# Kernel optimization log

Measured on AMD Instinct MI355X. Metric: run time of the kernel, lower is better.

Reference implementation:

```python
import jax, jax.numpy as jnp
import numpy as np

BN_EPS = 1e-5


def _weight_mlp(off, Wh, bh, Wo, bo):
    # off: [Nout, k, 2] relative neighbor offsets -> [Nout, k, 9] interp coeffs
    h = jax.nn.relu(off @ Wh + bh)
    return h @ Wo + bo


def _interp_conv(x, idx, off, Wk, bk, Wh, bh, Wo, bo):
    # x: [B, Cin, Nin]; idx: [Nout, k] neighbor indices into Nin; Wk: [Cout, Cin, 9]
    a = _weight_mlp(off, Wh, bh, Wo, bo)        # [Nout, k, 9]
    feats = x[:, :, idx]                         # gather -> [B, Cin, Nout, k]
    # dynamic filter: per-neighbor kernel = a @ Wk taps, contracted with features
    y = jnp.einsum('nkt,bcnk,oct->bon', a, feats, Wk)  # [B, Cout, Nout]
    return y + bk[None, :, None]


def _bn_relu(x, g, b):
    # BatchNorm1d over [B, C, N] using batch statistics (training-mode forward)
    mean = x.mean(axis=(0, 2), keepdims=True)
    var = x.var(axis=(0, 2), keepdims=True)
    xn = (x - mean) * jax.lax.rsqrt(var + BN_EPS)
    return jax.nn.relu(xn * g[None, :, None] + b[None, :, None])


def setup_inputs() -> dict:
    key = jax.random.key(0)
    ks = jax.random.split(key, 12)
    B, N1, N2, N3, K = 8, 50176, 12544, 3136, 9
    inp = {
        'x': jax.random.normal(ks[0], (B, 3, N1), jnp.float32),
        'nbr1': jax.random.randint(ks[1], (N2, K), 0, N1, jnp.int32),
        'off1': jax.random.normal(ks[2], (N2, K, 2), jnp.float32),
        'nbr2': jax.random.randint(ks[3], (N2, K), 0, N2, jnp.int32),
        'off2': jax.random.normal(ks[4], (N2, K, 2), jnp.float32),
        'pool_idx': jax.random.randint(ks[5], (N3, K), 0, N2, jnp.int32),
        'Wh': jax.random.normal(ks[6], (2, 32), jnp.float32) * 0.5,
        'bh': jnp.zeros((32,), jnp.float32),
        'Wo': jax.random.normal(ks[7], (32, 9), jnp.float32) * 0.2,
        'bo': jnp.zeros((9,), jnp.float32),
        'W1': jax.random.normal(ks[8], (32, 3, 9), jnp.float32) * 0.2,
        'b1': jnp.zeros((32,), jnp.float32),
        'W2': jax.random.normal(ks[9], (32, 32, 9), jnp.float32) * 0.06,
        'b2': jnp.zeros((32,), jnp.float32),
        'W3': jax.random.normal(ks[10], (64, 32, 9), jnp.float32) * 0.06,
        'b3': jnp.zeros((64,), jnp.float32),
        'g1': jnp.ones((32,), jnp.float32), 'be1': jnp.zeros((32,), jnp.float32),
        'g2': jnp.ones((32,), jnp.float32), 'be2': jnp.zeros((32,), jnp.float32),
        'g3': jnp.ones((64,), jnp.float32), 'be3': jnp.zeros((64,), jnp.float32),
    }
    return inp


def reference(x, nbr1, off1, nbr2, off2, pool_idx, Wh, bh, Wo, bo,
              W1, b1, W2, b2, W3, b3, g1, be1, g2, be2, g3, be3):
    x = _bn_relu(_interp_conv(x, nbr1, off1, W1, b1, Wh, bh, Wo, bo), g1, be1)
    x = _bn_relu(_interp_conv(x, nbr2, off2, W2, b2, Wh, bh, Wo, bo), g2, be2)
    x = _bn_relu(_interp_conv(x, nbr2, off2, W3, b3, Wh, bh, Wo, bo), g3, be3)
    # MaxPoolNG: max over irregular neighbor sets from level l2 -> l3
    x = x[:, :, pool_idx].max(axis=-1)           # [B, 64, N3]
    return x
```

## Files before the change

kernel.cpp:

```cpp
#include <hip/hip_runtime.h>
#include <math.h>

#define N1C 50176
#define N2C 12544
#define N3C 3136
#define NT_TILES (N2C * 8 / 64)

typedef __attribute__((ext_vector_type(8))) short bf16x8;
typedef __attribute__((ext_vector_type(4))) float f32x4;

__device__ __forceinline__ unsigned short f2bf(float f) {
    unsigned u = __builtin_bit_cast(unsigned, f);
    u += 0x7fffu + ((u >> 16) & 1u);
    return (unsigned short)(u >> 16);
}
__device__ __forceinline__ unsigned packbf(float a, float b) {
    return (unsigned)f2bf(a) | ((unsigned)f2bf(b) << 16);
}
__device__ __forceinline__ float bf2f(unsigned short u) {
    return __builtin_bit_cast(float, (unsigned)u << 16);
}
__device__ __forceinline__ float bflo(unsigned u) {
    return __builtin_bit_cast(float, u << 16);
}
__device__ __forceinline__ float bfhi(unsigned u) {
    return __builtin_bit_cast(float, u & 0xffff0000u);
}

#define TRB (N1C / 64)
#define MLB (2 * N2C * 9 / 256)
#define PWB 112

__device__ __forceinline__ void pad_one(int i, const float* __restrict__ W,
                                        unsigned short* __restrict__ Wp,
                                        int OC, int CIN, int KT) {
    int j = i & 7;
    int op = (i >> 3) & 31;
    int q = (i >> 8) & 3;
    int kt = (i >> 10) % KT;
    int g = i / (KT * 1024);
    int kp = kt * 32 + q * 8 + j;
    int t = kp / CIN, c = kp - t * CIN;
    int o = g * 32 + op;
    float v = (t < 9 && o < OC) ? W[(o * CIN + c) * 9 + t] : 0.f;
    Wp[i] = f2bf(v);
}

__global__ void prologue_kernel(const float* __restrict__ x, unsigned short* __restrict__ X0,
                                const float* __restrict__ off1, const float* __restrict__ off2,
                                const float* __restrict__ Wh, const float* __restrict__ bh,
                                const float* __restrict__ Wo, const float* __restrict__ bo,
                                float* __restrict__ A1, float* __restrict__ A2,
                                const float* __restrict__ W1, const float* __restrict__ W2,
                                const float* __restrict__ W3,
                                unsigned short* __restrict__ W1p, unsigned short* __restrict__ W2p,
                                unsigned short* __restrict__ W3p) {
    __shared__ float T[64][25];
    int blk = blockIdx.x;
    int tid = threadIdx.x;
    if (blk < TRB) {
        int n0 = blk * 64;
        for (int r = tid; r < 24 * 64; r += 256) {
            int cb = r >> 6;
            int nn = r & 63;
            T[nn][cb] = x[cb * N1C + n0 + nn];
        }
        __syncthreads();
        for (int w = tid; w < 64 * 24; w += 256) {
            int nn = w / 24;
            int u = w - nn * 24;
            X0[(n0 + nn) * 24 + u] = f2bf(T[nn][u]);
        }
    } else if (blk < TRB + MLB) {
        int idx = (blk - TRB) * 256 + tid;
        const float* offp;
        float* Ap;
        if (idx < N2C * 9) { offp = off1 + idx * 2; Ap = A1 + idx * 9; }
        else { int i2 = idx - N2C * 9; offp = off2 + i2 * 2; Ap = A2 + i2 * 9; }
        float o0 = offp[0], o1 = offp[1];
        float out[9];
#pragma unroll
        for (int t = 0; t < 9; t++) out[t] = bo[t];
#pragma unroll
        for (int h = 0; h < 32; h++) {
            float hv = fmaxf(o0 * Wh[h] + o1 * Wh[32 + h] + bh[h], 0.f);
#pragma unroll
            for (int t = 0; t < 9; t++) out[t] += hv * Wo[h * 9 + t];
        }
#pragma unroll
        for (int t = 0; t < 9; t++) Ap[t] = out[t];
    } else {
        int i = (blk - TRB - MLB) * 256 + tid;
        if (i < 1024) pad_one(i, W1, W1p, 32, 3, 1);
        else if (i < 10240) pad_one(i - 1024, W2, W2p, 32, 32, 9);
        else pad_one(i - 10240, W3, W3p, 64, 288 / 9, 9);
    }
}

template <int CIN, int MW, bool HAS_BN>
__global__ __launch_bounds__(256, 4)
void conv_kernel(const unsigned short* __restrict__ Xin,
                 const int* __restrict__ nbr,
                 const float* __restrict__ A,
                 const unsigned short* __restrict__ Wp,
                 const float* __restrict__ bias,
                 const float* __restrict__ bnsc,
                 const float* __restrict__ bnsh,
                 unsigned short* __restrict__ Yb,
                 double* __restrict__ Part) {
    constexpr int OC = MW * 16;
    constexpr int KREAL = 9 * CIN;
    constexpr int KROW = (KREAL + 31) & ~31;
    constexpr int KT = KROW / 32;
    constexpr int KSTR = KROW + 8;
    __shared__ alignas(16) short S[64 * KSTR];

    int tid = threadIdx.x;
    int tile = blockIdx.x;
    int n0 = tile * 8;

    if constexpr (KROW != KREAL) {
        for (int i = tid; i < 64 * KSTR; i += 256) S[i] = 0;
        __syncthreads();
    }

    if constexpr (CIN == 3) {
        if (tid < 192) {
            int nsub = tid / 24;
            int u = tid - nsub * 24;
            int b = u / 3, c = u - b * 3;
            int n = n0 + nsub;
            const int* nb = nbr + n * 9;
            const float* Ar = A + n * 81;
            float s[9];
#pragma unroll
            for (int t = 0; t < 9; t++) s[t] = 0.f;
#pragma unroll
            for (int k = 0; k < 9; k++) {
                float f = bf2f(Xin[nb[k] * 24 + u]);
#pragma unroll
                for (int t = 0; t < 9; t++) s[t] = fmaf(Ar[k * 9 + t], f, s[t]);
            }
            int col = nsub * 8 + b;
#pragma unroll
            for (int t = 0; t < 9; t++) S[col * KSTR + t * 3 + c] = (short)f2bf(s[t]);
        }
    } else {
        int wv4 = __builtin_amdgcn_readfirstlane(tid >> 6);
        int lane = tid & 63;
        int b = lane >> 3, c4 = lane & 7;
        float4 scv = {1.f, 1.f, 1.f, 1.f}, shv = {0.f, 0.f, 0.f, 0.f};
        if (HAS_BN) {
            scv = *(const float4*)&bnsc[4 * c4];
            shv = *(const float4*)&bnsh[4 * c4];
        }
        const uint2* Xd = (const uint2*)Xin;
        uint2 fu[18];
#pragma unroll
        for (int gg = 0; gg < 2; gg++)
#pragma unroll
            for (int k = 0; k < 9; k++) {
                int j = nbr[(n0 + wv4 * 2 + gg) * 9 + k];
                fu[gg * 9 + k] = Xd[(size_t)j * 64 + lane];
            }
#pragma unroll
        for (int gg = 0; gg < 2; gg++) {
            const float* Ar = A + (size_t)(n0 + wv4 * 2 + gg) * 81;
            float s0[9], s1[9], s2[9], s3[9];
#pragma unroll
            for (int t = 0; t < 9; t++) { s0[t] = 0.f; s1[t] = 0.f; s2[t] = 0.f; s3[t] = 0.f; }
#pragma unroll
            for (int k = 0; k < 9; k++) {
                uint2 u = fu[gg * 9 + k];
                float f0 = bflo(u.x), f1 = bfhi(u.x);
                float f2 = bflo(u.y), f3 = bfhi(u.y);
                if (HAS_BN) {
                    f0 = fmaxf(fmaf(f0, scv.x, shv.x), 0.f);
                    f1 = fmaxf(fmaf(f1, scv.y, shv.y), 0.f);
                    f2 = fmaxf(fmaf(f2, scv.z, shv.z), 0.f);
                    f3 = fmaxf(fmaf(f3, scv.w, shv.w), 0.f);
                }
#pragma unroll
                for (int t = 0; t < 9; t++) {
                    float a = Ar[k * 9 + t];
                    s0[t] = fmaf(a, f0, s0[t]);
                    s1[t] = fmaf(a, f1, s1[t]);
                    s2[t] = fmaf(a, f2, s2[t]);
                    s3[t] = fmaf(a, f3, s3[t]);
                }
            }
            int col = (wv4 * 2 + gg) * 8 + b;
            uint2* Srow = (uint2*)&S[col * KSTR];
#pragma unroll
            for (int t = 0; t < 9; t++) {
                uint2 pk;
                pk.x = packbf(s0[t], s1[t]);
                pk.y = packbf(s2[t], s3[t]);
                Srow[t * 8 + c4] = pk;
            }
        }
    }
    __syncthreads();

    int lane = tid & 63, wv = tid >> 6, q = lane >> 4, cl = lane & 15;
    int colg = wv * 16 + cl;

    const bf16x8* wf = (const bf16x8*)Wp;
    f32x4 acc[MW];
#pragma unroll
    for (int m = 0; m < MW; m++) acc[m] = (f32x4){0.f, 0.f, 0.f, 0.f};
#pragma unroll
    for (int kt = 0; kt < KT; kt++) {
        bf16x8 bfr = *(const bf16x8*)&S[colg * KSTR + kt * 32 + q * 8];
#pragma unroll
        for (int m = 0; m < MW; m++) {
            const bf16x8* wg = wf + (m >> 1) * (KT * 128);
            bf16x8 am = wg[(kt * 4 + q) * 32 + cl + (m & 1) * 16];
            acc[m] = __builtin_amdgcn_mfma_f32_16x16x32_bf16(am, bfr, acc[m], 0, 0, 0);
        }
    }
    __syncthreads();
    float (*redf)[2 * OC] = (float(*)[2 * OC])S;

    int C = tile * 64 + colg;
    float yv[4 * MW];
#pragma unroll
    for (int m = 0; m < MW; m++) {
#pragma unroll
        for (int i = 0; i < 4; i++) {
            int o = m * 16 + q * 4 + i;
            yv[m * 4 + i] = acc[m][i] + bias[o];
        }
        uint2 pk;
        pk.x = packbf(yv[m * 4 + 0], yv[m * 4 + 1]);
        pk.y = packbf(yv[m * 4 + 2], yv[m * 4 + 3]);
        *(uint2*)&Yb[(size_t)C * OC + m * 16 + q * 4] = pk;
    }
#pragma unroll
    for (int r = 0; r < 4 * MW; r++) {
        float ps = yv[r];
        float pq = yv[r] * yv[r];
#pragma unroll
        for (int d = 1; d < 16; d <<= 1) {
            ps += __shfl_xor(ps, d);
            pq += __shfl_xor(pq, d);
        }
        if (cl == 0) {
            int o = (r >> 2) * 16 + q * 4 + (r & 3);
            redf[wv][o] = ps;
            redf[wv][OC + o] = pq;
        }
    }
    __syncthreads();
    if (tid < 2 * OC) {
        double v = (double)redf[0][tid] + (double)redf[1][tid] +
                   (double)redf[2][tid] + (double)redf[3][tid];
        Part[(size_t)tid * NT_TILES + tile] = v;
    }
}

__global__ __launch_bounds__(256, 8)
void bn_reduce(const double* __restrict__ Part,
               const float* __restrict__ g, const float* __restrict__ be,
               float* __restrict__ sc, float* __restrict__ sh, int OC) {
    int o = blockIdx.x;
    int tid = threadIdx.x;
    const double* ps = Part + (size_t)o * NT_TILES;
    const double* pq = Part + (size_t)(OC + o) * NT_TILES;
    double s = 0.0, q = 0.0;
    for (int t = tid; t < NT_TILES; t += 256) {
        s += ps[t];
        q += pq[t];
    }
#pragma unroll
    for (int d = 1; d < 64; d <<= 1) {
        s += __shfl_xor(s, d);
        q += __shfl_xor(q, d);
    }
    __shared__ double red[8];
    int wv = tid >> 6;
    if ((tid & 63) == 0) { red[wv] = s; red[4 + wv] = q; }
    __syncthreads();
    if (tid == 0) {
        double S = red[0] + red[1] + red[2] + red[3];
        double Q = red[4] + red[5] + red[6] + red[7];
        double cnt = (double)N2C * 8.0;
        double mean = S / cnt;
        double var = Q / cnt - mean * mean;
        double rs = 1.0 / sqrt(var + 1e-5);
        double scale = (double)g[o] * rs;
        sc[o] = (float)scale;
        sh[o] = (float)((double)be[o] - mean * scale);
    }
}

__global__ __launch_bounds__(256, 8)
void pool_kernel(const unsigned short* __restrict__ Y3, const int* __restrict__ pidx,
                 const float* __restrict__ sc, const float* __restrict__ sh,
                 float* __restrict__ out) {
    int m0 = blockIdx.x * 2;
    int tid = threadIdx.x;
    int o2 = tid & 31;
    int b = tid >> 5;
    float s0 = sc[2 * o2], h0 = sh[2 * o2];
    float s1 = sc[2 * o2 + 1], h1 = sh[2 * o2 + 1];
    const unsigned* Y3u = (const unsigned*)Y3;
    int j0[9], j1[9];
#pragma unroll
    for (int k = 0; k < 9; k++) {
        j0[k] = pidx[m0 * 9 + k];
        j1[k] = pidx[m0 * 9 + 9 + k];
    }
    unsigned u0[9], u1[9];
#pragma unroll
    for (int k = 0; k < 9; k++) u0[k] = Y3u[(size_t)j0[k] * 256 + tid];
#pragma unroll
    for (int k = 0; k < 9; k++) u1[k] = Y3u[(size_t)j1[k] * 256 + tid];
    float a0 = 0.f, a1 = 0.f, c0 = 0.f, c1 = 0.f;
#pragma unroll
    for (int k = 0; k < 9; k++) {
        a0 = fmaxf(a0, fmaf(bflo(u0[k]), s0, h0));
        a1 = fmaxf(a1, fmaf(bfhi(u0[k]), s1, h1));
        c0 = fmaxf(c0, fmaf(bflo(u1[k]), s0, h0));
        c1 = fmaxf(c1, fmaf(bfhi(u1[k]), s1, h1));
    }
    float2 r0 = {a0, c0};
    float2 r1 = {a1, c1};
    *(float2*)(out + (size_t)(b * 64 + 2 * o2) * 3136 + m0) = r0;
    *(float2*)(out + (size_t)(b * 64 + 2 * o2 + 1) * 3136 + m0) = r1;
}

extern "C" void kernel_launch(void* const* d_in, const int* in_sizes, int n_in,
                              void* d_out, int out_size, void* d_ws, size_t ws_size,
                              hipStream_t stream) {
    const float* x    = (const float*)d_in[0];
    const int*   nbr1 = (const int*)d_in[1];
    const float* off1 = (const float*)d_in[2];
    const int*   nbr2 = (const int*)d_in[3];
    const float* off2 = (const float*)d_in[4];
    const int*   pidx = (const int*)d_in[5];
    const float* Wh   = (const float*)d_in[6];
    const float* bh   = (const float*)d_in[7];
    const float* Wo   = (const float*)d_in[8];
    const float* bo   = (const float*)d_in[9];
    const float* W1   = (const float*)d_in[10];
    const float* b1   = (const float*)d_in[11];
    const float* W2   = (const float*)d_in[12];
    const float* b2   = (const float*)d_in[13];
    const float* W3   = (const float*)d_in[14];
    const float* b3   = (const float*)d_in[15];
    const float* g1   = (const float*)d_in[16];
    const float* be1  = (const float*)d_in[17];
    const float* g2   = (const float*)d_in[18];
    const float* be2  = (const float*)d_in[19];
    const float* g3   = (const float*)d_in[20];
    const float* be3  = (const float*)d_in[21];

    char* ws = (char*)d_ws;
    size_t off = 0;
    auto alloc = [&](size_t bytes) -> void* {
        void* p = ws + off;
        off += (bytes + 255) & ~(size_t)255;
        return p;
    };
    unsigned short* X0b = (unsigned short*)alloc((size_t)N1C * 24 * 2);
    float* A1 = (float*)alloc((size_t)N2C * 81 * 4);
    float* A2 = (float*)alloc((size_t)N2C * 81 * 4);
    unsigned short* Y1b = (unsigned short*)alloc((size_t)N2C * 8 * 32 * 2);
    unsigned short* Y2b = (unsigned short*)alloc((size_t)N2C * 8 * 32 * 2);
    unsigned short* Y3b = (unsigned short*)alloc((size_t)N2C * 8 * 64 * 2);
    unsigned short* W1p = (unsigned short*)alloc(32 * 32 * 2);
    unsigned short* W2p = (unsigned short*)alloc(32 * 288 * 2);
    unsigned short* W3p = (unsigned short*)alloc(64 * 288 * 2);
    double* Part  = (double*)alloc((size_t)NT_TILES * 128 * 8);
    float*  scbuf = (float*)alloc(256 * 4);

    float* sc1 = scbuf;       float* sh1 = scbuf + 32;
    float* sc2 = scbuf + 64;  float* sh2 = scbuf + 96;
    float* sc3 = scbuf + 128; float* sh3 = scbuf + 192;

    prologue_kernel<<<TRB + MLB + PWB, 256, 0, stream>>>(
        x, X0b, off1, off2, Wh, bh, Wo, bo, A1, A2, W1, W2, W3, W1p, W2p, W3p);

    conv_kernel<3, 2, false><<<NT_TILES, 256, 0, stream>>>(
        X0b, nbr1, A1, W1p, b1, nullptr, nullptr, Y1b, Part);
    bn_reduce<<<32, 256, 0, stream>>>(Part, g1, be1, sc1, sh1, 32);

    conv_kernel<32, 2, true><<<NT_TILES, 256, 0, stream>>>(
        Y1b, nbr2, A2, W2p, b2, sc1, sh1, Y2b, Part);
    bn_reduce<<<32, 256, 0, stream>>>(Part, g2, be2, sc2, sh2, 32);

    conv_kernel<32, 4, true><<<NT_TILES, 256, 0, stream>>>(
        Y2b, nbr2, A2, W3p, b3, sc2, sh2, Y3b, Part);
    bn_reduce<<<64, 256, 0, stream>>>(Part, g3, be3, sc3, sh3, 64);

    pool_kernel<<<N3C / 2, 256, 0, stream>>>(Y3b, pidx, sc3, sh3, (float*)d_out);
}
```

Measured before the change: 192.3 us.

## Stage A coeffs in LDS, coalesce MLP stores, replace shuffle BN reduction

The prologue MLP now writes its 9 outputs per thread to shared memory and then stores the block's results contiguously, giving coalesced writes to A1/A2. The conv kernel cooperatively loads the block's 8×81 interpolation coefficients into LDS rather than having every lane read them from global memory. The per-channel BN sum and sum-of-squares reduction moves from a 16-lane xor-shuffle tree to staging fp32 outputs in LDS and doing a column-wise partial reduction. The cost is more LDS use and extra barriers, which may lower occupancy.

After: 189.7 us. No clear change (-1.4%).

```diff
diff --git a/kernel.cpp b/kernel.cpp
--- a/kernel.cpp
+++ b/kernel.cpp
@@ -55,7 +55,7 @@
                                 const float* __restrict__ W3,
                                 unsigned short* __restrict__ W1p, unsigned short* __restrict__ W2p,
                                 unsigned short* __restrict__ W3p) {
-    __shared__ float T[64][25];
+    __shared__ float U[2304];
     int blk = blockIdx.x;
     int tid = threadIdx.x;
     if (blk < TRB) {
@@ -63,20 +63,20 @@
         for (int r = tid; r < 24 * 64; r += 256) {
             int cb = r >> 6;
             int nn = r & 63;
-            T[nn][cb] = x[cb * N1C + n0 + nn];
+            U[nn * 25 + cb] = x[cb * N1C + n0 + nn];
         }
         __syncthreads();
         for (int w = tid; w < 64 * 24; w += 256) {
             int nn = w / 24;
             int u = w - nn * 24;
-            X0[(n0 + nn) * 24 + u] = f2bf(T[nn][u]);
+            X0[(n0 + nn) * 24 + u] = f2bf(U[nn * 25 + u]);
         }
     } else if (blk < TRB + MLB) {
-        int idx = (blk - TRB) * 256 + tid;
+        int bi = blk - TRB;
+        int idx = bi * 256 + tid;
         const float* offp;
-        float* Ap;
-        if (idx < N2C * 9) { offp = off1 + idx * 2; Ap = A1 + idx * 9; }
-        else { int i2 = idx - N2C * 9; offp = off2 + i2 * 2; Ap = A2 + i2 * 9; }
+        if (idx < N2C * 9) offp = off1 + idx * 2;
+        else offp = off2 + (idx - N2C * 9) * 2;
         float o0 = offp[0], o1 = offp[1];
         float out[9];
 #pragma unroll
@@ -88,12 +88,16 @@
             for (int t = 0; t < 9; t++) out[t] += hv * Wo[h * 9 + t];
         }
 #pragma unroll
-        for (int t = 0; t < 9; t++) Ap[t] = out[t];
+        for (int t = 0; t < 9; t++) U[tid * 9 + t] = out[t];
+        __syncthreads();
+        float* dst = (bi < 441) ? (A1 + (size_t)bi * 2304)
+                                : (A2 + (size_t)(bi - 441) * 2304);
+        for (int i = tid; i < 2304; i += 256) dst[i] = U[i];
     } else {
         int i = (blk - TRB - MLB) * 256 + tid;
         if (i < 1024) pad_one(i, W1, W1p, 32, 3, 1);
         else if (i < 10240) pad_one(i - 1024, W2, W2p, 32, 32, 9);
-        else pad_one(i - 10240, W3, W3p, 64, 288 / 9, 9);
+        else pad_one(i - 10240, W3, W3p, 64, 32, 9);
     }
 }
 
@@ -113,25 +117,32 @@
     constexpr int KROW = (KREAL + 31) & ~31;
     constexpr int KT = KROW / 32;
     constexpr int KSTR = KROW + 8;
-    __shared__ alignas(16) short S[64 * KSTR];
+    constexpr int PARTS = 256 / OC;
+    constexpr int PCOLS = 64 / PARTS;
+    constexpr int OSH = (OC == 32) ? 5 : 6;
+    constexpr int YSTR = OC + 4;
+    constexpr int SB1 = 64 * KSTR * 2;
+    constexpr int SB2 = 64 * YSTR * 4 + PARTS * 2 * OC * 4;
+    constexpr int SBYTES = SB1 > SB2 ? SB1 : SB2;
+    __shared__ alignas(16) char Sraw[SBYTES];
+    __shared__ float a_lds[8 * 81];
+    short* S = (short*)Sraw;
 
     int tid = threadIdx.x;
     int tile = blockIdx.x;
     int n0 = tile * 8;
 
-    if constexpr (KROW != KREAL) {
+    if constexpr (CIN == 3) {
         for (int i = tid; i < 64 * KSTR; i += 256) S[i] = 0;
+        for (int i = tid; i < 648; i += 256) a_lds[i] = A[(size_t)n0 * 81 + i];
         __syncthreads();
-    }
-
-    if constexpr (CIN == 3) {
         if (tid < 192) {
             int nsub = tid / 24;
             int u = tid - nsub * 24;
             int b = u / 3, c = u - b * 3;
             int n = n0 + nsub;
             const int* nb = nbr + n * 9;
-            const float* Ar = A + n * 81;
+            const float* Ar = a_lds + nsub * 81;
             float s[9];
 #pragma unroll
             for (int t = 0; t < 9; t++) s[t] = 0.f;
@@ -163,9 +174,11 @@
                 int j = nbr[(n0 + wv4 * 2 + gg) * 9 + k];
                 fu[gg * 9 + k] = Xd[(size_t)j * 64 + lane];
             }
+        for (int i = tid; i < 648; i += 256) a_lds[i] = A[(size_t)n0 * 81 + i];
+        __syncthreads();
 #pragma unroll
         for (int gg = 0; gg < 2; gg++) {
-            const float* Ar = A + (size_t)(n0 + wv4 * 2 + gg) * 81;
+            const float* Ar = a_lds + (wv4 * 2 + gg) * 81;
             float s0[9], s1[9], s2[9], s3[9];
 #pragma unroll
             for (int t = 0; t < 9; t++) { s0[t] = 0.f; s1[t] = 0.f; s2[t] = 0.f; s3[t] = 0.f; }
@@ -220,41 +233,40 @@
         }
     }
     __syncthreads();
-    float (*redf)[2 * OC] = (float(*)[2 * OC])S;
-
+
+    float* Yf = (float*)Sraw;
+    float* P2f = Yf + 64 * YSTR;
     int C = tile * 64 + colg;
-    float yv[4 * MW];
 #pragma unroll
     for (int m = 0; m < MW; m++) {
-#pragma unroll
-        for (int i = 0; i < 4; i++) {
-            int o = m * 16 + q * 4 + i;
-            yv[m * 4 + i] = acc[m][i] + bias[o];
-        }
+        f32x4 v;
+#pragma unroll
+        for (int i = 0; i < 4; i++) v[i] = acc[m][i] + bias[m * 16 + q * 4 + i];
+        *(f32x4*)&Yf[colg * YSTR + m * 16 + q * 4] = v;
         uint2 pk;
-        pk.x = packbf(yv[m * 4 + 0], yv[m * 4 + 1]);
-        pk.y = packbf(yv[m * 4 + 2], yv[m * 4 + 3]);
+        pk.x = packbf(v[0], v[1]);
+        pk.y = packbf(v[2], v[3]);
         *(uint2*)&Yb[(size_t)C * OC + m * 16 + q * 4] = pk;
     }
-#pragma unroll
-    for (int r = 0; r < 4 * MW; r++) {
-        float ps = yv[r];
-        float pq = yv[r] * yv[r];
-#pragma unroll
-        for (int d = 1; d < 16; d <<= 1) {
-            ps += __shfl_xor(ps, d);
-            pq += __shfl_xor(pq, d);
-        }
-        if (cl == 0) {
-            int o = (r >> 2) * 16 + q * 4 + (r & 3);
-            redf[wv][o] = ps;
-            redf[wv][OC + o] = pq;
-        }
+    __syncthreads();
+    {
+        int o = tid & (OC - 1);
+        int part = tid >> OSH;
+        float s = 0.f, qq = 0.f;
+#pragma unroll
+        for (int i = 0; i < PCOLS; i++) {
+            float y = Yf[(part * PCOLS + i) * YSTR + o];
+            s += y;
+            qq += y * y;
+        }
+        P2f[part * 2 * OC + o] = s;
+        P2f[part * 2 * OC + OC + o] = qq;
     }
     __syncthreads();
     if (tid < 2 * OC) {
-        double v = (double)redf[0][tid] + (double)redf[1][tid] +
-                   (double)redf[2][tid] + (double)redf[3][tid];
+        double v = 0.0;
+#pragma unroll
+        for (int p = 0; p < PARTS; p++) v += (double)P2f[p * 2 * OC + tid];
         Part[(size_t)tid * NT_TILES + tile] = v;
     }
 }
```
